# Kernel optimization log

Measured on AMD Instinct MI355X. Metric: run time of the kernel, lower is better.

## Reference

```python
import jax, jax.numpy as jnp
import numpy as np

N_NODES = {'movie': 50000, 'director': 10000, 'actor': 25000}
# relation name -> (src_type, dst_type, num_edges)
RELS = {'md': ('movie', 'director', 150000),
        'dm': ('director', 'movie', 150000),
        'ma': ('movie', 'actor', 300000),
        'am': ('actor', 'movie', 300000)}
F_IN, HID, HEADS, OUT = 1024, 256, 8, 4
HD = HID // HEADS  # 32 per-head dim


def setup_inputs() -> dict:
    key = jax.random.key(0)
    kit = iter(jax.random.split(key, 128))
    def nrm(shape, s):
        return jax.random.normal(next(kit), shape, jnp.float32) * s
    inp = {}
    for t, n in N_NODES.items():
        inp['x_' + t] = nrm((n, F_IN), 1.0)
    for rn, (st, dt, e) in RELS.items():
        inp['e_' + rn + '_src'] = jax.random.randint(next(kit), (e,), 0, N_NODES[st], dtype=jnp.int32)
        inp['e_' + rn + '_dst'] = jax.random.randint(next(kit), (e,), 0, N_NODES[dt], dtype=jnp.int32)
        inp['a_' + rn] = nrm((HEADS, HD, HD), 0.05)   # per-relation attention matrix
        inp['m_' + rn] = nrm((HEADS, HD, HD), 0.05)   # per-relation message matrix
        inp['p_' + rn] = jnp.ones((HEADS,), jnp.float32)  # relation priority
    for t in N_NODES:
        inp['W_in_' + t] = nrm((F_IN, HID), 0.02)
        inp['b_in_' + t] = jnp.zeros((HID,), jnp.float32)
        for nm in ('k', 'q', 'v'):
            inp['W' + nm + '_' + t] = nrm((HID, HID), 0.05)
            inp['b' + nm + '_' + t] = jnp.zeros((HID,), jnp.float32)
        inp['Wa_' + t] = nrm((HID, HID), 0.05)
        inp['ba_' + t] = jnp.zeros((HID,), jnp.float32)
        inp['skip_' + t] = jnp.array(1.0, jnp.float32)
    inp['W_out'] = nrm((HID, OUT), 0.05)
    inp['b_out'] = jnp.zeros((OUT,), jnp.float32)
    return inp


def _forward(p):
    # per-node-type input projection (the HGT.lin_dict step)
    h = {t: p['x_' + t] @ p['W_in_' + t] + p['b_in_' + t] for t in N_NODES}
    # per-type K/Q/V projections, reshaped to [N, H, D]
    def proj(nm):
        return {t: (h[t] @ p['W' + nm + '_' + t] + p['b' + nm + '_' + t]).reshape(-1, HEADS, HD)
                for t in N_NODES}
    k, q, v = proj('k'), proj('q'), proj('v')
    scale = 1.0 / np.sqrt(HD)
    # per-edge-type: gather, relation-transform, score
    buf = {t: [] for t in N_NODES}
    for rn, (st, dt, _) in RELS.items():
        si, di = p['e_' + rn + '_src'], p['e_' + rn + '_dst']
        ke = jnp.einsum('ehd,hdf->ehf', k[st][si], p['a_' + rn])  # [E,H,D]
        ve = jnp.einsum('ehd,hdf->ehf', v[st][si], p['m_' + rn])  # [E,H,D]
        al = (q[dt][di] * ke).sum(-1) * (p['p_' + rn] * scale)    # [E,H]
        buf[dt].append((di, al, ve))
    # destination-grouped segment softmax + scatter aggregation
    out = {}
    for t, n in N_NODES.items():
        di = jnp.concatenate([b[0] for b in buf[t]])
        al = jnp.concatenate([b[1] for b in buf[t]])
        ve = jnp.concatenate([b[2] for b in buf[t]])
        amax = jax.ops.segment_max(al, di, num_segments=n)        # [N,H]
        amax = jnp.where(jnp.isfinite(amax), amax, 0.0)
        ex = jnp.exp(al - amax[di])
        den = jax.ops.segment_sum(ex, di, num_segments=n)[di]
        w = ex / jnp.where(den > 0, den, 1.0)                     # [E,H]
        agg = jax.ops.segment_sum(w[:, :, None] * ve, di, num_segments=n).reshape(n, HID)
        o = jax.nn.gelu(agg @ p['Wa_' + t] + p['ba_' + t])
        beta = jax.nn.sigmoid(p['skip_' + t])                     # gated skip connection
        out[t] = beta * o + (1.0 - beta) * h[t]
    # final classifier on movie nodes
    return out['movie'] @ p['W_out'] + p['b_out']


def reference(x_movie, x_director, x_actor, e_md_src, e_md_dst, a_md, m_md, p_md, e_dm_src, e_dm_dst, a_dm, m_dm, p_dm, e_ma_src, e_ma_dst, a_ma, m_ma, p_ma, e_am_src, e_am_dst, a_am, m_am, p_am, W_in_movie, b_in_movie, Wk_movie, bk_movie, Wq_movie, bq_movie, Wv_movie, bv_movie, Wa_movie, ba_movie, skip_movie, W_in_director, b_in_director, Wk_director, bk_director, Wq_director, bq_director, Wv_director, bv_director, Wa_director, ba_director, skip_director, W_in_actor, b_in_actor, Wk_actor, bk_actor, Wq_actor, bq_actor, Wv_actor, bv_actor, Wa_actor, ba_actor, skip_actor, W_out, b_out):
    p = dict(locals())
    return _forward(p)
```

## Files before the change

### kernel.cpp

```cpp
#include <hip/hip_runtime.h>
#include <math.h>

#define NM 50000
#define ND 10000
#define NA 25000
#define E_DM 150000
#define E_AM 300000
#define E_TOT (E_DM + E_AM)
#define HID 256
#define HEADS 8
#define HD 32
#define FIN 1024
#define SCALE 0.17677669529663687f

typedef __attribute__((ext_vector_type(8))) short short8;
typedef __attribute__((ext_vector_type(4))) float f32x4;

typedef __attribute__((address_space(1))) const unsigned char gas_u8;
typedef __attribute__((address_space(3))) unsigned char las_u8;

__device__ __forceinline__ void gload16(const void* g, void* l) {
    gas_u8* gp = (gas_u8*)(unsigned long long)(uintptr_t)g;
    las_u8* lp = (las_u8*)(unsigned int)(uintptr_t)l;
    __builtin_amdgcn_global_load_lds((const __attribute__((address_space(1))) void*)gp,
                                     (__attribute__((address_space(3))) void*)lp, 16, 0, 0);
}

__device__ __forceinline__ unsigned int pk_bf16(float x, float y) {
    unsigned int a = __float_as_uint(x), b = __float_as_uint(y);
    a += 0x7FFFu + ((a >> 16) & 1u);
    b += 0x7FFFu + ((b >> 16) & 1u);
    return (a >> 16) | (b & 0xFFFF0000u);
}
__device__ __forceinline__ unsigned short to_bf16(float x) {
    unsigned int a = __float_as_uint(x);
    a += 0x7FFFu + ((a >> 16) & 1u);
    return (unsigned short)(a >> 16);
}
__device__ __forceinline__ float bf2f(unsigned short u) {
    return __uint_as_float(((unsigned int)u) << 16);
}

struct F4 { const float* W[4]; const float* b[4]; const float* a[4]; float* Wf[4]; float* bf[4]; };
__global__ void fold_w4(F4 f4) {
    int di = blockIdx.y;
    const float* W = f4.W[di]; const float* b = f4.b[di]; const float* a = f4.a[di];
    float* Wf = f4.Wf[di]; float* bf = f4.bf[di];
    int c = threadIdx.x;
    int h = c >> 5, f = c & 31;
    int r = blockIdx.x;
    float acc = 0.f;
    if (r < HID) {
        #pragma unroll
        for (int d = 0; d < HD; ++d)
            acc += W[r * HID + h * HD + d] * a[(h * HD + d) * HD + f];
        Wf[r * HID + c] = acc;
    } else {
        #pragma unroll
        for (int d = 0; d < HD; ++d)
            acc += b[h * HD + d] * a[(h * HD + d) * HD + f];
        bf[c] = acc;
    }
}

struct PDesc { const float* W; unsigned short* out; int K; int b0; };
struct PMulti { PDesc d[9]; int nd; };
__global__ void wt_pack(PMulti pm) {
    int bid = blockIdx.x; int di = 0;
    #pragma unroll
    for (int i = 1; i < 9; ++i) if (i < pm.nd && bid >= pm.d[i].b0) di = i;
    PDesc p = pm.d[di];
    int kstep = bid - p.b0;
    int t = threadIdx.x;
    #pragma unroll
    for (int i = 0; i < 32; ++i) {
        int idx = i * 256 + t;
        int n0 = idx >> 9, r = idx & 511, lane = r >> 3, j = r & 7;
        int k = kstep * 32 + (lane >> 4) * 8 + j;
        int c = n0 * 16 + (lane & 15);
        p.out[(size_t)kstep * 8192 + idx] = to_bf16(p.W[(size_t)k * HID + c]);
    }
}

struct GDesc {
    const void* A; const unsigned short* Bt; const float* bias; void* C;
    const void* hskip; const float* gate; int M; int K; int epi; int obf; int abf; int b0;
};
struct GMulti { GDesc d[5]; int nd; };

#define GBM 128

__launch_bounds__(512, 4)
__global__ void gemm_mfma(GMulti mu) {
    __shared__ unsigned short sB[2][16 * 512];
    __shared__ unsigned short sA[2][8 * 512];

    int bid = blockIdx.x;
    int di = 0;
    #pragma unroll
    for (int i = 1; i < 5; ++i)
        if (i < mu.nd && bid >= mu.d[i].b0) di = i;
    GDesc g = mu.d[di];
    int bm = (bid - g.b0) * GBM;
    int M = g.M, K = g.K;

    int t = threadIdx.x;
    int lane = t & 63;
    int w = t >> 6;
    int wr = w >> 2, wc = w & 3;
    int l16 = lane & 15;

    int arow = bm + w * 16 + l16;
    const float* Ap = nullptr;
    const unsigned short* Abp = nullptr;
    if (g.abf) Abp = (const unsigned short*)g.A + (size_t)min(arow, M - 1) * K + ((lane >> 4) * 8);
    else Ap = (arow < M) ? ((const float*)g.A + (size_t)arow * K + ((lane >> 4) * 8)) : nullptr;
    int aoff = w * 512 + lane * 8;

    f32x4 acc[4][4];
    #pragma unroll
    for (int m = 0; m < 4; ++m)
        #pragma unroll
        for (int n = 0; n < 4; ++n) acc[m][n] = (f32x4)(0.f);

    int nk = K >> 5;
    {
        const unsigned short* gB = g.Bt;
        gload16(gB + w * 512 + lane * 8, &sB[0][w * 512]);
        gload16(gB + (w + 8) * 512 + lane * 8, &sB[0][(w + 8) * 512]);
        if (g.abf) {
            gload16(Abp, &sA[0][w * 512]);
        } else {
            uint4 pk = make_uint4(0u, 0u, 0u, 0u);
            if (Ap) {
                float4 a0 = *(const float4*)(Ap);
                float4 a1 = *(const float4*)(Ap + 4);
                pk = make_uint4(pk_bf16(a0.x, a0.y), pk_bf16(a0.z, a0.w),
                                pk_bf16(a1.x, a1.y), pk_bf16(a1.z, a1.w));
            }
            *(uint4*)&sA[0][aoff] = pk;
        }
    }
    __syncthreads();

    int cur = 0;
    for (int ks = 0; ks < nk; ++ks) {
        int nxt = cur ^ 1;
        bool pf = (ks + 1 < nk);
        float4 f0, f1;
        if (pf) {
            const unsigned short* gB = g.Bt + (size_t)(ks + 1) * 8192;
            gload16(gB + w * 512 + lane * 8, &sB[nxt][w * 512]);
            gload16(gB + (w + 8) * 512 + lane * 8, &sB[nxt][(w + 8) * 512]);
            if (g.abf) {
                gload16(Abp + (ks + 1) * 32, &sA[nxt][w * 512]);
            } else if (Ap) {
                f0 = *(const float4*)(Ap + (ks + 1) * 32);
                f1 = *(const float4*)(Ap + (ks + 1) * 32 + 4);
            }
        }
        short8 af[4], bfr[4];
        #pragma unroll
        for (int m = 0; m < 4; ++m)
            af[m] = *(const short8*)&sA[cur][(wr * 4 + m) * 512 + lane * 8];
        #pragma unroll
        for (int n = 0; n < 4; ++n)
            bfr[n] = *(const short8*)&sB[cur][(wc * 4 + n) * 512 + lane * 8];
        #pragma unroll
        for (int m = 0; m < 4; ++m)
            #pragma unroll
            for (int n = 0; n < 4; ++n)
                acc[m][n] = __builtin_amdgcn_mfma_f32_16x16x32_bf16(af[m], bfr[n], acc[m][n], 0, 0, 0);
        if (pf && !g.abf) {
            uint4 pk = make_uint4(0u, 0u, 0u, 0u);
            if (Ap) pk = make_uint4(pk_bf16(f0.x, f0.y), pk_bf16(f0.z, f0.w),
                                    pk_bf16(f1.x, f1.y), pk_bf16(f1.z, f1.w));
            *(uint4*)&sA[nxt][aoff] = pk;
        }
        __syncthreads();
        cur = nxt;
    }

    float beta = 0.f;
    if (g.epi) beta = 1.f / (1.f + expf(-g.gate[0]));
    #pragma unroll
    for (int m = 0; m < 4; ++m) {
        int r0 = bm + wr * 64 + m * 16 + ((lane >> 4) << 2);
        #pragma unroll
        for (int n = 0; n < 4; ++n) {
            int col = wc * 64 + n * 16 + l16;
            #pragma unroll
            for (int j = 0; j < 4; ++j) {
                int grow = r0 + j;
                if (grow >= M) continue;
                float v = acc[m][n][j] + g.bias[col];
                if (g.epi) {
                    float x = v;
                    float gl = 0.5f * x * (1.f + tanhf(0.7978845608028654f * (x + 0.044715f * x * x * x)));
                    float hv = bf2f(((const unsigned short*)g.hskip)[(size_t)grow * HID + col]);
                    v = beta * gl + (1.f - beta) * hv;
                }
                if (g.obf) ((unsigned short*)g.C)[(size_t)grow * HID + col] = to_bf16(v);
                else ((float*)g.C)[(size_t)grow * HID + col] = v;
            }
        }
    }
}

__global__ void hist_deg(const int* __restrict__ dA, const int* __restrict__ dB,
                         int* __restrict__ deg) {
    int i = blockIdx.x * 256 + threadIdx.x;
    if (i < E_DM) atomicAdd(&deg[dA[i]], 1);
    else if (i < E_TOT) atomicAdd(&deg[dB[i - E_DM]], 1);
}

__global__ void scan_pass1(const int* __restrict__ deg, int* __restrict__ bsum) {
    __shared__ int s[256];
    int b = blockIdx.x, t = threadIdx.x;
    int i = b * 256 + t;
    int v = (i < NM) ? deg[i] : 0;
    s[t] = v; __syncthreads();
    for (int off = 128; off > 0; off >>= 1) {
        if (t < off) s[t] += s[t + off];
        __syncthreads();
    }
    if (t == 0) bsum[b] = s[0];
}

__global__ void scan_pass2(const int* __restrict__ bsum, int* __restrict__ boff, int nb) {
    __shared__ int s[256];
    int t = threadIdx.x;
    int v = (t < nb) ? bsum[t] : 0;
    s[t] = v; __syncthreads();
    for (int off = 1; off < 256; off <<= 1) {
        int x = (t >= off) ? s[t - off] : 0;
        __syncthreads();
        s[t] += x;
        __syncthreads();
    }
    if (t < nb) boff[t] = s[t] - v;
}

__global__ void scan_pass3(const int* __restrict__ deg, const int* __restrict__ boff,
                           int* __restrict__ rowptr, int* __restrict__ cursor) {
    __shared__ int s[256];
    int b = blockIdx.x, t = threadIdx.x, i = b * 256 + t;
    int v = (i < NM) ? deg[i] : 0;
    s[t] = v; __syncthreads();
    for (int off = 1; off < 256; off <<= 1) {
        int x = (t >= off) ? s[t - off] : 0;
        __syncthreads();
        s[t] += x;
        __syncthreads();
    }
    int excl = s[t] - v + boff[b];
    if (i < NM) { rowptr[i] = excl; cursor[i] = excl; }
    if (i == 0) rowptr[NM] = E_TOT;
}

__global__ void fill_adj(const int* __restrict__ sA, const int* __restrict__ dA,
                         const int* __restrict__ sB, const int* __restrict__ dB,
                         int* __restrict__ cursor, int* __restrict__ adj) {
    int i = blockIdx.x * 256 + threadIdx.x;
    int d, entry;
    if (i < E_DM)      { d = dA[i];        entry = sA[i]; }
    else if (i < E_TOT){ int j = i - E_DM; d = dB[j]; entry = (sB[j] + ND) | (1 << 16); }
    else return;
    int pos = atomicAdd(&cursor[d], 1);
    adj[pos] = entry;
}

__launch_bounds__(256)
__global__ void agg_fused(const int* __restrict__ rowptr, const int* __restrict__ adj,
                          const float* __restrict__ q, const unsigned short* __restrict__ kt_all,
                          const unsigned short* __restrict__ vt_all,
                          const float* __restrict__ p_dm, const float* __restrict__ p_am,
                          float* __restrict__ agg) {
    int d = blockIdx.x * 4 + (threadIdx.x >> 6);
    if (d >= NM) return;
    int lane = threadIdx.x & 63;
    int h = lane >> 3;
    int start = rowptr[d], end = rowptr[d + 1];
    float4 qv = *(const float4*)(q + (size_t)d * HID + lane * 4);
    float pr0 = p_dm[h] * SCALE, pr1 = p_am[h] * SCALE;
    float m = -INFINITY, den = 0.f, a0 = 0.f, a1 = 0.f, a2 = 0.f, a3 = 0.f;
    for (int i = start; i < end; ++i) {
        int e = adj[i];
        int sr = e & 0xFFFF;
        uint2 ku = *(const uint2*)(kt_all + (size_t)sr * HID + lane * 4);
        float k0 = __uint_as_float(ku.x << 16), k1 = __uint_as_float(ku.x & 0xFFFF0000u);
        float k2 = __uint_as_float(ku.y << 16), k3 = __uint_as_float(ku.y & 0xFFFF0000u);
        float prod = qv.x * k0 + qv.y * k1 + qv.z * k2 + qv.w * k3;
        prod += __shfl_xor(prod, 1);
        prod += __shfl_xor(prod, 2);
        prod += __shfl_xor(prod, 4);
        float a = prod * ((e >> 16) ? pr1 : pr0);
        float mn = fmaxf(m, a);
        float c  = __expf(m - mn);
        float ex = __expf(a - mn);
        uint2 vu = *(const uint2*)(vt_all + (size_t)sr * HID + lane * 4);
        float v0 = __uint_as_float(vu.x << 16), v1 = __uint_as_float(vu.x & 0xFFFF0000u);
        float v2 = __uint_as_float(vu.y << 16), v3 = __uint_as_float(vu.y & 0xFFFF0000u);
        den = den * c + ex;
        a0 = a0 * c + ex * v0; a1 = a1 * c + ex * v1;
        a2 = a2 * c + ex * v2; a3 = a3 * c + ex * v3;
        m = mn;
    }
    float inv = (end > start) ? 1.f / den : 0.f;
    *(float4*)(agg + (size_t)d * HID + lane * 4) = make_float4(a0 * inv, a1 * inv, a2 * inv, a3 * inv);
}

__launch_bounds__(256)
__global__ void classifier(const float* __restrict__ X, const float* __restrict__ W,
                           const float* __restrict__ b, float* __restrict__ out, int M) {
    int t = threadIdx.x, lane = t & 63;
    int wid = blockIdx.x * 4 + (t >> 6);
    int nw = gridDim.x * 4;
    float w0[4], w1[4], w2[4], w3[4];
    #pragma unroll
    for (int j = 0; j < 4; ++j) {
        float4 wv = *(const float4*)(W + (lane * 4 + j) * 4);
        w0[j] = wv.x; w1[j] = wv.y; w2[j] = wv.z; w3[j] = wv.w;
    }
    float b0 = b[0], b1 = b[1], b2 = b[2], b3 = b[3];
    for (int row = wid; row < M; row += nw) {
        float4 x = *(const float4*)(X + (size_t)row * HID + lane * 4);
        float s0 = x.x * w0[0] + x.y * w0[1] + x.z * w0[2] + x.w * w0[3];
        float s1 = x.x * w1[0] + x.y * w1[1] + x.z * w1[2] + x.w * w1[3];
        float s2 = x.x * w2[0] + x.y * w2[1] + x.z * w2[2] + x.w * w2[3];
        float s3 = x.x * w3[0] + x.y * w3[1] + x.z * w3[2] + x.w * w3[3];
        #pragma unroll
        for (int off = 32; off > 0; off >>= 1) {
            s0 += __shfl_xor(s0, off); s1 += __shfl_xor(s1, off);
            s2 += __shfl_xor(s2, off); s3 += __shfl_xor(s3, off);
        }
        if (lane == 0) {
            float4 o = make_float4(s0 + b0, s1 + b1, s2 + b2, s3 + b3);
            *(float4*)(out + (size_t)row * 4) = o;
        }
    }
}

extern "C" void kernel_launch(void* const* d_in, const int* in_sizes, int n_in,
                              void* d_out, int out_size, void* d_ws, size_t ws_size,
                              hipStream_t stream) {
    (void)in_sizes; (void)n_in; (void)out_size; (void)ws_size;
    const float* x_movie    = (const float*)d_in[0];
    const float* x_director = (const float*)d_in[1];
    const float* x_actor    = (const float*)d_in[2];
    const int*   e_dm_src = (const int*)d_in[8];
    const int*   e_dm_dst = (const int*)d_in[9];
    const float* a_dm     = (const float*)d_in[10];
    const float* m_dm     = (const float*)d_in[11];
    const float* p_dm     = (const float*)d_in[12];
    const int*   e_am_src = (const int*)d_in[18];
    const int*   e_am_dst = (const int*)d_in[19];
    const float* a_am     = (const float*)d_in[20];
    const float* m_am     = (const float*)d_in[21];
    const float* p_am     = (const float*)d_in[22];
    const float* W_in_m = (const float*)d_in[23];
    const float* b_in_m = (const float*)d_in[24];
    const float* Wq_m   = (const float*)d_in[27];
    const float* bq_m   = (const float*)d_in[28];
    const float* Wa_m   = (const float*)d_in[31];
    const float* ba_m   = (const float*)d_in[32];
    const float* skip_m = (const float*)d_in[33];
    const float* W_in_d = (const float*)d_in[34];
    const float* b_in_d = (const float*)d_in[35];
    const float* Wk_d   = (const float*)d_in[36];
    const float* bk_d   = (const float*)d_in[37];
    const float* Wv_d   = (const float*)d_in[40];
    const float* bv_d   = (const float*)d_in[41];
    const float* W_in_a = (const float*)d_in[45];
    const float* b_in_a = (const float*)d_in[46];
    const float* Wk_a   = (const float*)d_in[47];
    const float* bk_a   = (const float*)d_in[48];
    const float* Wv_a   = (const float*)d_in[51];
    const float* bv_a   = (const float*)d_in[52];
    const float* W_out  = (const float*)d_in[56];
    const float* b_out  = (const float*)d_in[57];

    char* base = (char*)d_ws;
    size_t off = 0;
    auto alloc = [&](size_t bytes) -> void* {
        void* p = base + off;
        off = (off + bytes + 255) & ~(size_t)255;
        return p;
    };
    unsigned short* h_m = (unsigned short*)alloc((size_t)NM * HID * 2);
    unsigned short* h_d = (unsigned short*)alloc((size_t)ND * HID * 2);
    unsigned short* h_a = (unsigned short*)alloc((size_t)NA * HID * 2);
    float* q_m    = (float*)alloc((size_t)NM * HID * 4);
    float* out_m  = (float*)alloc((size_t)NM * HID * 4);
    float* agg    = (float*)alloc((size_t)NM * HID * 4);
    unsigned short* kt_all = (unsigned short*)alloc((size_t)(ND + NA) * HID * 2);
    unsigned short* vt_all = (unsigned short*)alloc((size_t)(ND + NA) * HID * 2);
    float* Wf     = (float*)alloc(4 * (size_t)HID * HID * 4);
    float* bf     = (float*)alloc(4 * (size_t)HID * 4);
    int* deg      = (int*)alloc(NM * 4);
    int* rowptr   = (int*)alloc((NM + 1) * 4);
    int* cursor   = (int*)alloc(NM * 4);
    int* bsum     = (int*)alloc(256 * 4);
    int* boff     = (int*)alloc(256 * 4);
    int* adj      = (int*)alloc((size_t)E_TOT * 4);
    unsigned short* Bt_in_m = (unsigned short*)alloc((size_t)256 * 1024 * 2);
    unsigned short* Bt_in_d = (unsigned short*)alloc((size_t)256 * 1024 * 2);
    unsigned short* Bt_in_a = (unsigned short*)alloc((size_t)256 * 1024 * 2);
    unsigned short* Bt_q_m  = (unsigned short*)alloc((size_t)256 * 256 * 2);
    unsigned short* Bt_k_dm = (unsigned short*)alloc((size_t)256 * 256 * 2);
    unsigned short* Bt_v_dm = (unsigned short*)alloc((size_t)256 * 256 * 2);
    unsigned short* Bt_k_am = (unsigned short*)alloc((size_t)256 * 256 * 2);
    unsigned short* Bt_v_am = (unsigned short*)alloc((size_t)256 * 256 * 2);
    unsigned short* Bt_a_m  = (unsigned short*)alloc((size_t)256 * 256 * 2);

    unsigned short* kt_dm = kt_all;
    unsigned short* kt_am = kt_all + (size_t)ND * HID;
    unsigned short* vt_dm = vt_all;
    unsigned short* vt_am = vt_all + (size_t)ND * HID;

    float* Wf_k_dm = Wf + 0 * HID * HID;  float* bf_k_dm = bf + 0 * HID;
    float* Wf_v_dm = Wf + 1 * HID * HID;  float* bf_v_dm = bf + 1 * HID;
    float* Wf_k_am = Wf + 2 * HID * HID;  float* bf_k_am = bf + 2 * HID;
    float* Wf_v_am = Wf + 3 * HID * HID;  float* bf_v_am = bf + 3 * HID;

    hipMemsetAsync(deg, 0, NM * sizeof(int), stream);
    hist_deg<<<(E_TOT + 255) / 256, 256, 0, stream>>>(e_dm_dst, e_am_dst, deg);
    int nb = (NM + 255) / 256;
    scan_pass1<<<nb, 256, 0, stream>>>(deg, bsum);
    scan_pass2<<<1, 256, 0, stream>>>(bsum, boff, nb);
    scan_pass3<<<nb, 256, 0, stream>>>(deg, boff, rowptr, cursor);
    fill_adj<<<(E_TOT + 255) / 256, 256, 0, stream>>>(e_dm_src, e_dm_dst, e_am_src, e_am_dst,
                                                      cursor, adj);

    {
        F4 f4{};
        f4.W[0] = Wk_d; f4.b[0] = bk_d; f4.a[0] = a_dm; f4.Wf[0] = Wf_k_dm; f4.bf[0] = bf_k_dm;
        f4.W[1] = Wv_d; f4.b[1] = bv_d; f4.a[1] = m_dm; f4.Wf[1] = Wf_v_dm; f4.bf[1] = bf_v_dm;
        f4.W[2] = Wk_a; f4.b[2] = bk_a; f4.a[2] = a_am; f4.Wf[2] = Wf_k_am; f4.bf[2] = bf_k_am;
        f4.W[3] = Wv_a; f4.b[3] = bv_a; f4.a[3] = m_am; f4.Wf[3] = Wf_v_am; f4.bf[3] = bf_v_am;
        fold_w4<<<dim3(257, 4), 256, 0, stream>>>(f4);
    }
    {
        PMulti pm{};
        pm.nd = 9;
        int b0 = 0;
        pm.d[0] = {W_in_m,  Bt_in_m, FIN, b0}; b0 += 32;
        pm.d[1] = {W_in_d,  Bt_in_d, FIN, b0}; b0 += 32;
        pm.d[2] = {W_in_a,  Bt_in_a, FIN, b0}; b0 += 32;
        pm.d[3] = {Wq_m,    Bt_q_m,  HID, b0}; b0 += 8;
        pm.d[4] = {Wf_k_dm, Bt_k_dm, HID, b0}; b0 += 8;
        pm.d[5] = {Wf_v_dm, Bt_v_dm, HID, b0}; b0 += 8;
        pm.d[6] = {Wf_k_am, Bt_k_am, HID, b0}; b0 += 8;
        pm.d[7] = {Wf_v_am, Bt_v_am, HID, b0}; b0 += 8;
        pm.d[8] = {Wa_m,    Bt_a_m,  HID, b0}; b0 += 8;
        wt_pack<<<b0, 256, 0, stream>>>(pm);
    }

    int bm_m = (NM + GBM - 1) / GBM;
    int bm_d = (ND + GBM - 1) / GBM;
    int bm_a = (NA + GBM - 1) / GBM;

    {
        GMulti mu{};
        mu.nd = 3;
        mu.d[0] = {x_movie,    Bt_in_m, b_in_m, h_m, nullptr, nullptr, NM, FIN, 0, 1, 0, 0};
        mu.d[1] = {x_director, Bt_in_d, b_in_d, h_d, nullptr, nullptr, ND, FIN, 0, 1, 0, bm_m};
        mu.d[2] = {x_actor,    Bt_in_a, b_in_a, h_a, nullptr, nullptr, NA, FIN, 0, 1, 0, bm_m + bm_d};
        gemm_mfma<<<bm_m + bm_d + bm_a, 512, 0, stream>>>(mu);
    }
    {
        GMulti mu{};
        mu.nd = 5;
        int b0 = 0;
        mu.d[0] = {h_m, Bt_q_m,  bq_m,    q_m,   nullptr, nullptr, NM, HID, 0, 0, 1, b0}; b0 += bm_m;
        mu.d[1] = {h_d, Bt_k_dm, bf_k_dm, kt_dm, nullptr, nullptr, ND, HID, 0, 1, 1, b0}; b0 += bm_d;
        mu.d[2] = {h_d, Bt_v_dm, bf_v_dm, vt_dm, nullptr, nullptr, ND, HID, 0, 1, 1, b0}; b0 += bm_d;
        mu.d[3] = {h_a, Bt_k_am, bf_k_am, kt_am, nullptr, nullptr, NA, HID, 0, 1, 1, b0}; b0 += bm_a;
        mu.d[4] = {h_a, Bt_v_am, bf_v_am, vt_am, nullptr, nullptr, NA, HID, 0, 1, 1, b0}; b0 += bm_a;
        gemm_mfma<<<b0, 512, 0, stream>>>(mu);
    }

    agg_fused<<<(NM + 3) / 4, 256, 0, stream>>>(rowptr, adj, q_m, kt_all, vt_all, p_dm, p_am, agg);

    {
        GMulti mu{};
        mu.nd = 1;
        mu.d[0] = {agg, Bt_a_m, ba_m, out_m, h_m, skip_m, NM, HID, 1, 0, 0, 0};
        gemm_mfma<<<bm_m, 512, 0, stream>>>(mu);
    }

    classifier<<<256, 256, 0, stream>>>(out_m, W_out, b_out, (float*)d_out, NM);
}
```

Before: 424.7 us.

## Halve GEMM row tile to 64 and remap warps to 16x128 output strips

The MFMA GEMM block tile shrinks from 128 to 64 rows. Each of the 8 warps now computes a 16-row by 128-column strip with 8 accumulators instead of a 4x4 grid of 16x16 tiles. For fp32 A input, the staging is redistributed so every thread loads one float4 per k-step, with row indices clamped instead of null-checked. The aim is more blocks across the large M dimensions, higher occupancy (launch bounds raised to 6, smaller LDS) and lower register pressure. The cost is that each B tile is reused across half as many rows, so B is loaded from LDS and global memory relatively more often.

```diff
diff --git a/kernel.cpp b/kernel.cpp
--- a/kernel.cpp
+++ b/kernel.cpp
@@ -88,12 +88,12 @@
 };
 struct GMulti { GDesc d[5]; int nd; };
 
-#define GBM 128
-
-__launch_bounds__(512, 4)
+#define GBM 64
+
+__launch_bounds__(512, 6)
 __global__ void gemm_mfma(GMulti mu) {
     __shared__ unsigned short sB[2][16 * 512];
-    __shared__ unsigned short sA[2][8 * 512];
+    __shared__ unsigned short sA[2][4 * 512];
 
     int bid = blockIdx.x;
     int di = 0;
@@ -107,21 +107,29 @@
     int t = threadIdx.x;
     int lane = t & 63;
     int w = t >> 6;
-    int wr = w >> 2, wc = w & 3;
+    int wp = w >> 1;
+    int ch = w & 1;
     int l16 = lane & 15;
 
-    int arow = bm + w * 16 + l16;
+    int slot = t >> 1;
+    int ss_ = slot >> 6;
+    int sl  = slot & 63;
+    int arow_f = bm + ss_ * 16 + (sl & 15);
+    int ak0    = (sl >> 4) * 8 + (t & 1) * 4;
     const float* Ap = nullptr;
     const unsigned short* Abp = nullptr;
-    if (g.abf) Abp = (const unsigned short*)g.A + (size_t)min(arow, M - 1) * K + ((lane >> 4) * 8);
-    else Ap = (arow < M) ? ((const float*)g.A + (size_t)arow * K + ((lane >> 4) * 8)) : nullptr;
-    int aoff = w * 512 + lane * 8;
-
-    f32x4 acc[4][4];
-    #pragma unroll
-    for (int m = 0; m < 4; ++m)
-        #pragma unroll
-        for (int n = 0; n < 4; ++n) acc[m][n] = (f32x4)(0.f);
+    if (g.abf) {
+        if (w < 4) {
+            int r = bm + w * 16 + l16;
+            Abp = (const unsigned short*)g.A + (size_t)min(r, M - 1) * K + ((lane >> 4) * 8);
+        }
+    } else {
+        Ap = (const float*)g.A + (size_t)min(arow_f, M - 1) * K + ak0;
+    }
+
+    f32x4 acc[8];
+    #pragma unroll
+    for (int n = 0; n < 8; ++n) acc[n] = (f32x4)(0.f);
 
     int nk = K >> 5;
     {
@@ -129,16 +137,11 @@
         gload16(gB + w * 512 + lane * 8, &sB[0][w * 512]);
         gload16(gB + (w + 8) * 512 + lane * 8, &sB[0][(w + 8) * 512]);
         if (g.abf) {
-            gload16(Abp, &sA[0][w * 512]);
+            if (w < 4) gload16(Abp, &sA[0][w * 512]);
         } else {
-            uint4 pk = make_uint4(0u, 0u, 0u, 0u);
-            if (Ap) {
-                float4 a0 = *(const float4*)(Ap);
-                float4 a1 = *(const float4*)(Ap + 4);
-                pk = make_uint4(pk_bf16(a0.x, a0.y), pk_bf16(a0.z, a0.w),
-                                pk_bf16(a1.x, a1.y), pk_bf16(a1.z, a1.w));
-            }
-            *(uint4*)&sA[0][aoff] = pk;
+            float4 f = *(const float4*)(Ap);
+            uint2 pk = make_uint2(pk_bf16(f.x, f.y), pk_bf16(f.z, f.w));
+            *(uint2*)&sA[0][slot * 8 + (t & 1) * 4] = pk;
         }
     }
     __syncthreads();
@@ -147,35 +150,28 @@
     for (int ks = 0; ks < nk; ++ks) {
         int nxt = cur ^ 1;
         bool pf = (ks + 1 < nk);
-        float4 f0, f1;
+        float4 f;
         if (pf) {
             const unsigned short* gB = g.Bt + (size_t)(ks + 1) * 8192;
             gload16(gB + w * 512 + lane * 8, &sB[nxt][w * 512]);
             gload16(gB + (w + 8) * 512 + lane * 8, &sB[nxt][(w + 8) * 512]);
             if (g.abf) {
-                gload16(Abp + (ks + 1) * 32, &sA[nxt][w * 512]);
-            } else if (Ap) {
-                f0 = *(const float4*)(Ap + (ks + 1) * 32);
-                f1 = *(const float4*)(Ap + (ks + 1) * 32 + 4);
+                if (w < 4) gload16(Abp + (ks + 1) * 32, &sA[nxt][w * 512]);
+            } else {
+                f = *(const float4*)(Ap + (ks + 1) * 32);
             }
         }
-        short8 af[4], bfr[4];
-        #pragma unroll
-        for (int m = 0; m < 4; ++m)
-            af[m] = *(const short8*)&sA[cur][(wr * 4 + m) * 512 + lane * 8];
-        #pragma unroll
-        for (int n = 0; n < 4; ++n)
-            bfr[n] = *(const short8*)&sB[cur][(wc * 4 + n) * 512 + lane * 8];
-        #pragma unroll
-        for (int m = 0; m < 4; ++m)
-            #pragma unroll
-            for (int n = 0; n < 4; ++n)
-                acc[m][n] = __builtin_amdgcn_mfma_f32_16x16x32_bf16(af[m], bfr[n], acc[m][n], 0, 0, 0);
+        short8 af = *(const short8*)&sA[cur][(wp * 64 + lane) * 8];
+        short8 bfr[8];
+        #pragma unroll
+        for (int n = 0; n < 8; ++n)
+            bfr[n] = *(const short8*)&sB[cur][((ch * 8 + n) * 64 + lane) * 8];
+        #pragma unroll
+        for (int n = 0; n < 8; ++n)
+            acc[n] = __builtin_amdgcn_mfma_f32_16x16x32_bf16(af, bfr[n], acc[n], 0, 0, 0);
         if (pf && !g.abf) {
-            uint4 pk = make_uint4(0u, 0u, 0u, 0u);
-            if (Ap) pk = make_uint4(pk_bf16(f0.x, f0.y), pk_bf16(f0.z, f0.w),
-                                    pk_bf16(f1.x, f1.y), pk_bf16(f1.z, f1.w));
-            *(uint4*)&sA[nxt][aoff] = pk;
+            uint2 pk = make_uint2(pk_bf16(f.x, f.y), pk_bf16(f.z, f.w));
+            *(uint2*)&sA[nxt][slot * 8 + (t & 1) * 4] = pk;
         }
         __syncthreads();
         cur = nxt;
@@ -183,26 +179,23 @@
 
     float beta = 0.f;
     if (g.epi) beta = 1.f / (1.f + expf(-g.gate[0]));
-    #pragma unroll
-    for (int m = 0; m < 4; ++m) {
-        int r0 = bm + wr * 64 + m * 16 + ((lane >> 4) << 2);
-        #pragma unroll
-        for (int n = 0; n < 4; ++n) {
-            int col = wc * 64 + n * 16 + l16;
-            #pragma unroll
-            for (int j = 0; j < 4; ++j) {
-                int grow = r0 + j;
-                if (grow >= M) continue;
-                float v = acc[m][n][j] + g.bias[col];
-                if (g.epi) {
-                    float x = v;
-                    float gl = 0.5f * x * (1.f + tanhf(0.7978845608028654f * (x + 0.044715f * x * x * x)));
-                    float hv = bf2f(((const unsigned short*)g.hskip)[(size_t)grow * HID + col]);
-                    v = beta * gl + (1.f - beta) * hv;
-                }
-                if (g.obf) ((unsigned short*)g.C)[(size_t)grow * HID + col] = to_bf16(v);
-                else ((float*)g.C)[(size_t)grow * HID + col] = v;
+    int r0 = bm + wp * 16 + ((lane >> 4) << 2);
+    #pragma unroll
+    for (int n = 0; n < 8; ++n) {
+        int col = ch * 128 + n * 16 + l16;
+        #pragma unroll
+        for (int j = 0; j < 4; ++j) {
+            int grow = r0 + j;
+            if (grow >= M) continue;
+            float v = acc[n][j] + g.bias[col];
+            if (g.epi) {
+                float x = v;
+                float gl = 0.5f * x * (1.f + tanhf(0.7978845608028654f * (x + 0.044715f * x * x * x)));
+                float hv = bf2f(((const unsigned short*)g.hskip)[(size_t)grow * HID + col]);
+                v = beta * gl + (1.f - beta) * hv;
             }
+            if (g.obf) ((unsigned short*)g.C)[(size_t)grow * HID + col] = to_bf16(v);
+            else ((float*)g.C)[(size_t)grow * HID + col] = v;
         }
     }
 }
```

New measurement: 416.7 us. No clear change (-1.9%).
